# Optimization experiments

Measured on AMD Instinct MI355X. Metric: run time of the kernel, lower is better.

The kernel has to match this reference:

```python
import jax, jax.numpy as jnp
import numpy as np

GRID = 16
N = GRID * GRID          # num_nodes = 256
D = 64                   # embed_dim
SPARSITY = 0.8
BATCH = 2048


def setup_inputs() -> dict:
    key = jax.random.key(0)
    ks = jax.random.split(key, 11)
    s1 = 1.0 / np.sqrt(D)          # fan_in of per-node Linears
    s2 = 1.0 / np.sqrt(N * D)      # fan_in of global_pool first Linear
    x = jax.random.normal(ks[0], (BATCH, N * D), dtype=jnp.float32)
    adj_param = jax.random.normal(ks[1], (N, N), dtype=jnp.float32) * 0.1
    W1 = jax.random.uniform(ks[2], (N, D, D), minval=-s1, maxval=s1, dtype=jnp.float32)
    b1 = jax.random.uniform(ks[3], (N, D), minval=-s1, maxval=s1, dtype=jnp.float32)
    W2 = jax.random.uniform(ks[4], (N, D, D), minval=-s1, maxval=s1, dtype=jnp.float32)
    b2 = jax.random.uniform(ks[5], (N, D), minval=-s1, maxval=s1, dtype=jnp.float32)
    gpW1 = jax.random.uniform(ks[6], (N * D, D), minval=-s2, maxval=s2, dtype=jnp.float32)
    gpb1 = jax.random.uniform(ks[7], (D,), minval=-s2, maxval=s2, dtype=jnp.float32)
    gpW2 = jax.random.uniform(ks[8], (D, D // 2), minval=-s1, maxval=s1, dtype=jnp.float32)
    gpb2 = jax.random.uniform(ks[9], (D // 2,), minval=-s1, maxval=s1, dtype=jnp.float32)
    return {"x": x, "adj_param": adj_param, "W1": W1, "b1": b1, "W2": W2, "b2": b2,
            "gpW1": gpW1, "gpb1": gpb1, "gpW2": gpW2, "gpb2": gpb2}


def _adjacency(adj_param):
    adj = jax.nn.sigmoid(adj_param)
    # threshold = sorted(flat adj)[int(sparsity * N*N)], then hard-threshold, then zero diagonal
    thr = jnp.sort(adj.reshape(-1))[int(SPARSITY * N * N)]
    adj = adj * (adj > thr)
    return adj * (1.0 - jnp.eye(N, dtype=adj.dtype))


def reference(x, adj_param, W1, b1, W2, b2, gpW1, gpb1, gpW2, gpb2):
    B = x.shape[0]
    adj = _adjacency(adj_param)
    xn = x.reshape(B, N, D)                                    # [B, N, D]
    # per-node distinct MLP == grouped GEMM with weights [N, D, D]
    h = jax.nn.relu(jnp.einsum('bnd,nde->bne', xn, W1) + b1)   # [B, N, D]
    node = jnp.einsum('bnd,nde->bne', h, W2) + b2              # [B, N, D]
    # adjacency-weighted neighbor sum: mixed[b,i] = sum_j adj[i,j] * node[b,j]
    mixed = jnp.einsum('ij,bjd->bid', adj, node)               # [B, N, D]
    final = 0.5 * mixed + 0.5 * node                           # residual mix
    g = jax.nn.relu(final.reshape(B, N * D) @ gpW1 + gpb1)     # [B, D]
    out = g @ gpW2 + gpb2                                      # [B, D//2]
    return out, adj
```

## Files before the change

### kernel.cpp

```cpp
#include <hip/hip_runtime.h>
#include <math.h>

typedef unsigned int uint;
typedef unsigned short ushort;
typedef short short8 __attribute__((ext_vector_type(8)));
typedef float f32x4 __attribute__((ext_vector_type(4)));

#define B_ 2048
#define N_ 256
#define D_ 64
#define ND_ 16384
#define NN_ 65536
#define KIDX_ 52428u
#define NGROUPS 32

#define WS_W1T    ((size_t)0)
#define WS_W2T    ((size_t)2*1024*1024)
#define WS_EFF    ((size_t)4*1024*1024)
#define WS_GPARTS ((size_t)8*1024*1024)
#define WS_SCAL   ((size_t)24*1024*1024)

__device__ __forceinline__ ushort f2bf(float f) {
    uint u = __float_as_uint(f);
    u += 0x7fffu + ((u >> 16) & 1u);
    return (ushort)(u >> 16);
}
__device__ __forceinline__ float bf2f(ushort u) { return __uint_as_float(((uint)u) << 16); }

__device__ __forceinline__ float sigmoid_exact(float a) {
    float t = (float)exp(-(double)a);
    return 1.0f / (1.0f + t);
}

__device__ __forceinline__ int wfrag_off(int e, int k) {
    return ((((e >> 4) * 2 + (k >> 5)) * 4 + ((k >> 3) & 3)) * 16 + (e & 15)) * 8 + (k & 7);
}

__device__ __forceinline__ int afrag_off(int jl, int i) {
    return (((((jl >> 4) * 8 + (i >> 5)) * 4 + ((i >> 3) & 3)) * 16) + (jl & 15)) * 8 + (i & 7);
}

__global__ __launch_bounds__(1024) void k_cvt_radix(const float* __restrict__ W1,
                                                    const float* __restrict__ W2,
                                                    const float* __restrict__ adj_param,
                                                    ushort* __restrict__ W1f,
                                                    ushort* __restrict__ W2f,
                                                    uint* __restrict__ scal) {
    __shared__ uint SH[16390] __attribute__((aligned(16)));
    int bid = blockIdx.x, tid = threadIdx.x;

    if (bid != 0) {
        int q = tid >> 8, t = tid & 255;
        int m = (bid - 1) * 4 + q;
        ushort* P = (ushort*)SH + q * 4096;
        const float* src = (m < 256) ? W1 + (size_t)m * 4096 : W2 + (size_t)(m - 256) * 4096;
#pragma unroll
        for (int i = 0; i < 16; i++) {
            int idx = i * 256 + t;
            int k = idx >> 6, e = idx & 63;
            P[wfrag_off(e, k)] = f2bf(src[idx]);
        }
        __syncthreads();
        ushort* dst = (m < 256) ? W1f + (size_t)m * 4096 : W2f + (size_t)(m - 256) * 4096;
#pragma unroll
        for (int i = 0; i < 2; i++)
            ((uint4*)dst)[i * 256 + t] = ((const uint4*)P)[i * 256 + t];
        return;
    }

    uint* histL = SH;
    uint* wsum = SH + 16384;
    uint* bc = SH + 16388;
    int lane = tid & 63;
    uint prefix = 0;
    uint rank = KIDX_;
    const uint4* pv = (const uint4*)adj_param;
#pragma unroll 1
    for (int pass = 0; pass < 4; pass++) {
        int shift = 24 - 8 * pass;
        for (int i = tid; i < 256 * 64; i += 1024) histL[i] = 0u;
        __syncthreads();
#pragma unroll 1
        for (int i = 0; i < 16; i++) {
            uint4 b4 = pv[i * 1024 + tid];
#pragma unroll
            for (int c = 0; c < 4; c++) {
                uint bits = (c == 0) ? b4.x : (c == 1) ? b4.y : (c == 2) ? b4.z : b4.w;
                uint key = bits ^ ((bits & 0x80000000u) ? 0xFFFFFFFFu : 0x80000000u);
                bool cand = (pass == 0) || ((key >> (32 - 8 * pass)) == prefix);
                if (cand) atomicAdd(&histL[(((key >> shift) & 0xffu) << 6) + lane], 1u);
            }
        }
        __syncthreads();
        uint s0 = 0, sc = 0;
        if (tid < 256) {
#pragma unroll
            for (int l = 0; l < 64; l++) s0 += histL[(tid << 6) + ((l + tid) & 63)];
            sc = s0;
#pragma unroll
            for (int o = 1; o < 64; o <<= 1) {
                uint t2 = __shfl_up(sc, o, 64);
                if ((tid & 63) >= o) sc += t2;
            }
            if ((tid & 63) == 63) wsum[tid >> 6] = sc;
        }
        __syncthreads();
        if (tid < 256) {
            uint base = 0;
#pragma unroll
            for (int w = 0; w < 4; w++)
                if (w < (tid >> 6)) base += wsum[w];
            uint incl = base + sc;
            uint excl = incl - s0;
            if (excl <= rank && rank < incl) {
                bc[0] = (prefix << 8) | (uint)tid;
                bc[1] = rank - excl;
            }
        }
        __syncthreads();
        prefix = bc[0];
        rank = bc[1];
        __syncthreads();
    }
    if (tid == 0) {
        uint key = prefix;
        uint bits = (key & 0x80000000u) ? (key ^ 0x80000000u) : ~key;
        scal[0] = __float_as_uint(sigmoid_exact(__uint_as_float(bits)));
    }
}

__global__ __launch_bounds__(256) void k_threff(const float* __restrict__ adj_param,
                                                const uint* __restrict__ scal,
                                                const float* __restrict__ gpW1,
                                                float* __restrict__ adj_out,
                                                ushort* __restrict__ effF) {
    __shared__ ushort adjS[16384] __attribute__((aligned(16)));
    __shared__ ushort Bf[16384] __attribute__((aligned(16)));
    int d = blockIdx.x, jt = blockIdx.y, tid = threadIdx.x;
    float thr = __uint_as_float(scal[0]);

    {
        int jl = tid & 63;
        int jglob = jt * 64 + jl;
        int wrow = tid >> 6;
#pragma unroll 1
        for (int i = 0; i < 16; i++) {
            float p[4];
#pragma unroll
            for (int u = 0; u < 4; u++)
                p[u] = adj_param[(size_t)((i * 4 + u) * 4 + wrow) * 256 + jglob];
#pragma unroll
            for (int u = 0; u < 4; u++) {
                int ir = (i * 4 + u) * 4 + wrow;
                float s = sigmoid_exact(p[u]);
                float v = (s > thr && ir != jglob) ? s : 0.0f;
                adjS[afrag_off(jl, ir)] = f2bf(v);
                if (d == 0) adj_out[(size_t)ir * 256 + jglob] = v;
            }
        }
    }
#pragma unroll
    for (int t = 0; t < 16; t++) {
        int idx = t * 256 + tid;
        int i = idx >> 4;
        int f4 = idx & 15;
        float4 v = *(const float4*)(gpW1 + ((size_t)i * 64 + d) * 64 + f4 * 4);
        int slab = i >> 6, il = i & 63, e0 = f4 * 4;
        Bf[slab * 4096 + wfrag_off(e0 + 0, il)] = f2bf(v.x);
        Bf[slab * 4096 + wfrag_off(e0 + 1, il)] = f2bf(v.y);
        Bf[slab * 4096 + wfrag_off(e0 + 2, il)] = f2bf(v.z);
        Bf[slab * 4096 + wfrag_off(e0 + 3, il)] = f2bf(v.w);
    }
    __syncthreads();
    int wid = tid >> 6, lane = tid & 63, quad = lane >> 4, l16 = lane & 15;
    f32x4 acc[4];
#pragma unroll
    for (int nt = 0; nt < 4; nt++) acc[nt] = (f32x4){0.f, 0.f, 0.f, 0.f};
#pragma unroll
    for (int ks8 = 0; ks8 < 8; ks8++) {
        short8 af = *(const short8*)&adjS[((((wid * 8 + ks8) * 4 + quad) * 16 + l16)) * 8];
        int slab = ks8 >> 1, ks = ks8 & 1;
#pragma unroll
        for (int nt = 0; nt < 4; nt++) {
            short8 bf = *(const short8*)&Bf[slab * 4096 + (((nt * 2 + ks) * 4 + quad) * 16 + l16) * 8];
            acc[nt] = __builtin_amdgcn_mfma_f32_16x16x32_bf16(af, bf, acc[nt], 0, 0, 0);
        }
    }
#pragma unroll
    for (int nt = 0; nt < 4; nt++) {
        int e = nt * 16 + l16;
#pragma unroll
        for (int r = 0; r < 4; r++) {
            int j = jt * 64 + wid * 16 + quad * 4 + r;
            float w = gpW1[((size_t)j * 64 + d) * 64 + e];
            float eff = 0.5f * (acc[nt][r] + w);
            effF[(size_t)j * 4096 + wfrag_off(e, d)] = f2bf(eff);
        }
    }
}

__global__ __launch_bounds__(256, 4) void k_fused(const float* __restrict__ x,
                                                  const ushort* __restrict__ W1f,
                                                  const ushort* __restrict__ W2f,
                                                  const ushort* __restrict__ effF,
                                                  const float* __restrict__ b1,
                                                  const float* __restrict__ b2,
                                                  float* __restrict__ gparts) {
    __shared__ ushort Wf1[4096] __attribute__((aligned(16)));
    __shared__ ushort Wf2[4096] __attribute__((aligned(16)));
    __shared__ ushort Ef[4096] __attribute__((aligned(16)));
    __shared__ ushort St[4][16 * 72];
    int tid = threadIdx.x;
    int g = blockIdx.x, bt = blockIdx.y;
    int wid = tid >> 6, lane = tid & 63, quad = lane >> 4, l16 = lane & 15;
    int rbase = bt * 64 + wid * 16;
    ushort* Sw = &St[wid][0];
    const float* xrow = x + (size_t)(rbase + l16) * ND_ + quad * 8;

    int n0 = g * 8;
    uint4 w1a = ((const uint4*)(W1f + (size_t)n0 * 4096))[tid];
    uint4 w1b = ((const uint4*)(W1f + (size_t)n0 * 4096))[256 + tid];
    uint4 w2a = ((const uint4*)(W2f + (size_t)n0 * 4096))[tid];
    uint4 w2b = ((const uint4*)(W2f + (size_t)n0 * 4096))[256 + tid];
    uint4 ea  = ((const uint4*)(effF + (size_t)n0 * 4096))[tid];
    uint4 eb  = ((const uint4*)(effF + (size_t)n0 * 4096))[256 + tid];
    float4 xr0, xr1, xr2, xr3;
    {
        const float* xp = xrow + (size_t)n0 * 64;
        xr0 = *(const float4*)(xp);
        xr1 = *(const float4*)(xp + 4);
        xr2 = *(const float4*)(xp + 32);
        xr3 = *(const float4*)(xp + 36);
    }
    float b1n[4], b2n[4];
#pragma unroll
    for (int nt = 0; nt < 4; nt++) {
        b1n[nt] = b1[n0 * 64 + nt * 16 + l16];
        b2n[nt] = b2[n0 * 64 + nt * 16 + l16];
    }
    ((uint4*)Wf1)[tid] = w1a;  ((uint4*)Wf1)[256 + tid] = w1b;
    ((uint4*)Wf2)[tid] = w2a;  ((uint4*)Wf2)[256 + tid] = w2b;
    ((uint4*)Ef)[tid]  = ea;   ((uint4*)Ef)[256 + tid]  = eb;

    f32x4 accg[4];
#pragma unroll
    for (int nt = 0; nt < 4; nt++) accg[nt] = (f32x4){0.f, 0.f, 0.f, 0.f};

    __syncthreads();

#pragma unroll 1
    for (int nl = 0; nl < 8; nl++) {
        short8 fa0, fa1;
        {
            short8 a;
            a[0] = (short)f2bf(xr0.x); a[1] = (short)f2bf(xr0.y);
            a[2] = (short)f2bf(xr0.z); a[3] = (short)f2bf(xr0.w);
            a[4] = (short)f2bf(xr1.x); a[5] = (short)f2bf(xr1.y);
            a[6] = (short)f2bf(xr1.z); a[7] = (short)f2bf(xr1.w);
            fa0 = a;
            short8 b;
            b[0] = (short)f2bf(xr2.x); b[1] = (short)f2bf(xr2.y);
            b[2] = (short)f2bf(xr2.z); b[3] = (short)f2bf(xr2.w);
            b[4] = (short)f2bf(xr3.x); b[5] = (short)f2bf(xr3.y);
            b[6] = (short)f2bf(xr3.z); b[7] = (short)f2bf(xr3.w);
            fa1 = b;
        }
        float bias1[4], bias2[4];
#pragma unroll
        for (int nt = 0; nt < 4; nt++) { bias1[nt] = b1n[nt]; bias2[nt] = b2n[nt]; }

        if (nl < 7) {
            int nn = g * 8 + nl + 1;
            w1a = ((const uint4*)(W1f + (size_t)nn * 4096))[tid];
            w1b = ((const uint4*)(W1f + (size_t)nn * 4096))[256 + tid];
            w2a = ((const uint4*)(W2f + (size_t)nn * 4096))[tid];
            w2b = ((const uint4*)(W2f + (size_t)nn * 4096))[256 + tid];
            ea  = ((const uint4*)(effF + (size_t)nn * 4096))[tid];
            eb  = ((const uint4*)(effF + (size_t)nn * 4096))[256 + tid];
            const float* xp = xrow + (size_t)nn * 64;
            xr0 = *(const float4*)(xp);
            xr1 = *(const float4*)(xp + 4);
            xr2 = *(const float4*)(xp + 32);
            xr3 = *(const float4*)(xp + 36);
#pragma unroll
            for (int nt = 0; nt < 4; nt++) {
                b1n[nt] = b1[nn * 64 + nt * 16 + l16];
                b2n[nt] = b2[nn * 64 + nt * 16 + l16];
            }
        }

        f32x4 acc[4];
#pragma unroll
        for (int nt = 0; nt < 4; nt++) acc[nt] = (f32x4){0.f, 0.f, 0.f, 0.f};
#pragma unroll
        for (int nt = 0; nt < 4; nt++) {
            short8 bf = *(const short8*)&Wf1[(((nt * 2 + 0) * 4 + quad) * 16 + l16) * 8];
            acc[nt] = __builtin_amdgcn_mfma_f32_16x16x32_bf16(fa0, bf, acc[nt], 0, 0, 0);
        }
#pragma unroll
        for (int nt = 0; nt < 4; nt++) {
            short8 bf = *(const short8*)&Wf1[(((nt * 2 + 1) * 4 + quad) * 16 + l16) * 8];
            acc[nt] = __builtin_amdgcn_mfma_f32_16x16x32_bf16(fa1, bf, acc[nt], 0, 0, 0);
        }
#pragma unroll
        for (int nt = 0; nt < 4; nt++)
#pragma unroll
            for (int r = 0; r < 4; r++) {
                float h = fmaxf(acc[nt][r] + bias1[nt], 0.0f);
                Sw[(quad * 4 + r) * 72 + nt * 16 + l16] = f2bf(h);
            }
        f32x4 acc2[4];
#pragma unroll
        for (int nt = 0; nt < 4; nt++) acc2[nt] = (f32x4){0.f, 0.f, 0.f, 0.f};
#pragma unroll
        for (int ks = 0; ks < 2; ks++) {
            short8 a2 = *(const short8*)&Sw[l16 * 72 + ks * 32 + quad * 8];
#pragma unroll
            for (int nt = 0; nt < 4; nt++) {
                short8 bf = *(const short8*)&Wf2[(((nt * 2 + ks) * 4 + quad) * 16 + l16) * 8];
                acc2[nt] = __builtin_amdgcn_mfma_f32_16x16x32_bf16(a2, bf, acc2[nt], 0, 0, 0);
            }
        }
#pragma unroll
        for (int nt = 0; nt < 4; nt++)
#pragma unroll
            for (int r = 0; r < 4; r++) {
                float v = acc2[nt][r] + bias2[nt];
                Sw[(quad * 4 + r) * 72 + nt * 16 + l16] = f2bf(v);
            }
#pragma unroll
        for (int ks = 0; ks < 2; ks++) {
            short8 a3 = *(const short8*)&Sw[l16 * 72 + ks * 32 + quad * 8];
#pragma unroll
            for (int nt = 0; nt < 4; nt++) {
                short8 bf = *(const short8*)&Ef[(((nt * 2 + ks) * 4 + quad) * 16 + l16) * 8];
                accg[nt] = __builtin_amdgcn_mfma_f32_16x16x32_bf16(a3, bf, accg[nt], 0, 0, 0);
            }
        }

        if (nl < 7) {
            __syncthreads();
            ((uint4*)Wf1)[tid] = w1a;  ((uint4*)Wf1)[256 + tid] = w1b;
            ((uint4*)Wf2)[tid] = w2a;  ((uint4*)Wf2)[256 + tid] = w2b;
            ((uint4*)Ef)[tid]  = ea;   ((uint4*)Ef)[256 + tid]  = eb;
            __syncthreads();
        }
    }

    float* gp = gparts + ((size_t)g * B_ + bt * 64) * 64;
#pragma unroll
    for (int nt = 0; nt < 4; nt++)
#pragma unroll
        for (int r = 0; r < 4; r++) {
            int b_loc = wid * 16 + quad * 4 + r;
            int e = nt * 16 + l16;
            gp[b_loc * 64 + e] = accg[nt][r];
        }
}

__global__ __launch_bounds__(256) void k_gp2(const float* __restrict__ gparts,
                                             const float* __restrict__ gpb1,
                                             const float* __restrict__ gpW2,
                                             const float* __restrict__ gpb2,
                                             float* __restrict__ out) {
    __shared__ float gs[4][64];
    int b0 = blockIdx.x * 4, tid = threadIdx.x;
    int r = tid >> 6, e = tid & 63;
    float s = gpb1[e];
#pragma unroll
    for (int p = 0; p < NGROUPS; p++)
        s += gparts[((size_t)p * B_ + b0 + r) * 64 + e];
    gs[r][e] = fmaxf(s, 0.0f);
    __syncthreads();
    if (tid < 128) {
        int rr = tid >> 5, o = tid & 31;
        float a = gpb2[o];
#pragma unroll 8
        for (int k2 = 0; k2 < 64; k2++) a += gs[rr][k2] * gpW2[k2 * 32 + o];
        out[(size_t)(b0 + rr) * 32 + o] = a;
    }
}

extern "C" void kernel_launch(void* const* d_in, const int* in_sizes, int n_in,
                              void* d_out, int out_size, void* d_ws, size_t ws_size,
                              hipStream_t stream) {
    const float* x = (const float*)d_in[0];
    const float* adj_param = (const float*)d_in[1];
    const float* W1 = (const float*)d_in[2];
    const float* b1 = (const float*)d_in[3];
    const float* W2 = (const float*)d_in[4];
    const float* b2 = (const float*)d_in[5];
    const float* gpW1 = (const float*)d_in[6];
    const float* gpb1 = (const float*)d_in[7];
    const float* gpW2 = (const float*)d_in[8];
    const float* gpb2 = (const float*)d_in[9];

    float* out = (float*)d_out;
    float* adj_out = (float*)d_out + NN_;

    char* ws = (char*)d_ws;
    ushort* W1f = (ushort*)(ws + WS_W1T);
    ushort* W2f = (ushort*)(ws + WS_W2T);
    ushort* effF = (ushort*)(ws + WS_EFF);
    float* gparts = (float*)(ws + WS_GPARTS);
    uint* scal = (uint*)(ws + WS_SCAL);

    k_cvt_radix<<<129, 1024, 0, stream>>>(W1, W2, adj_param, W1f, W2f, scal);
    k_threff<<<dim3(64, 4), 256, 0, stream>>>(adj_param, scal, gpW1, adj_out, effF);
    k_fused<<<dim3(NGROUPS, 32), 256, 0, stream>>>(x, W1f, W2f, effF, b1, b2, gparts);
    k_gp2<<<512, 256, 0, stream>>>(gparts, gpb1, gpW2, gpb2, out);
}
```

Baseline: 280.4 us.

## Read per-node MFMA weight fragments directly from global instead of LDS staging

The fused kernel no longer stages each node's W1, W2 and effective-pool weight fragments through shared memory. Each wave now loads its bf16 B-fragments straight from global memory, relying on L1/L2 to serve the copies that the four waves share. This removes the two block barriers and the LDS store traffic on every node iteration, and roughly halves shared-memory use. Biases for the block's eight nodes are loaded into shared memory once up front. The trade-off is redundant global/L1 traffic per wave, and the next node's weights are no longer prefetched, so their load latency is exposed unless other waves hide it.

Result: slower. 288.7 us (+2.9%).

```diff
diff --git a/kernel.cpp b/kernel.cpp
--- a/kernel.cpp
+++ b/kernel.cpp
@@ -206,10 +206,8 @@
                                                   const float* __restrict__ b1,
                                                   const float* __restrict__ b2,
                                                   float* __restrict__ gparts) {
-    __shared__ ushort Wf1[4096] __attribute__((aligned(16)));
-    __shared__ ushort Wf2[4096] __attribute__((aligned(16)));
-    __shared__ ushort Ef[4096] __attribute__((aligned(16)));
     __shared__ ushort St[4][16 * 72];
+    __shared__ float Bs[2][8][64];
     int tid = threadIdx.x;
     int g = blockIdx.x, bt = blockIdx.y;
     int wid = tid >> 6, lane = tid & 63, quad = lane >> 4, l16 = lane & 15;
@@ -217,30 +215,25 @@
     ushort* Sw = &St[wid][0];
     const float* xrow = x + (size_t)(rbase + l16) * ND_ + quad * 8;
 
-    int n0 = g * 8;
-    uint4 w1a = ((const uint4*)(W1f + (size_t)n0 * 4096))[tid];
-    uint4 w1b = ((const uint4*)(W1f + (size_t)n0 * 4096))[256 + tid];
-    uint4 w2a = ((const uint4*)(W2f + (size_t)n0 * 4096))[tid];
-    uint4 w2b = ((const uint4*)(W2f + (size_t)n0 * 4096))[256 + tid];
-    uint4 ea  = ((const uint4*)(effF + (size_t)n0 * 4096))[tid];
-    uint4 eb  = ((const uint4*)(effF + (size_t)n0 * 4096))[256 + tid];
+    {
+        const float* b1g = b1 + (size_t)g * 512;
+        const float* b2g = b2 + (size_t)g * 512;
+        ((float*)Bs[0])[tid] = b1g[tid];
+        ((float*)Bs[0])[256 + tid] = b1g[256 + tid];
+        ((float*)Bs[1])[tid] = b2g[tid];
+        ((float*)Bs[1])[256 + tid] = b2g[256 + tid];
+    }
+
+    int lo = quad * 128 + l16 * 8;
+
     float4 xr0, xr1, xr2, xr3;
     {
-        const float* xp = xrow + (size_t)n0 * 64;
+        const float* xp = xrow + (size_t)(g * 8) * 64;
         xr0 = *(const float4*)(xp);
         xr1 = *(const float4*)(xp + 4);
         xr2 = *(const float4*)(xp + 32);
         xr3 = *(const float4*)(xp + 36);
     }
-    float b1n[4], b2n[4];
-#pragma unroll
-    for (int nt = 0; nt < 4; nt++) {
-        b1n[nt] = b1[n0 * 64 + nt * 16 + l16];
-        b2n[nt] = b2[n0 * 64 + nt * 16 + l16];
-    }
-    ((uint4*)Wf1)[tid] = w1a;  ((uint4*)Wf1)[256 + tid] = w1b;
-    ((uint4*)Wf2)[tid] = w2a;  ((uint4*)Wf2)[256 + tid] = w2b;
-    ((uint4*)Ef)[tid]  = ea;   ((uint4*)Ef)[256 + tid]  = eb;
 
     f32x4 accg[4];
 #pragma unroll
@@ -250,6 +243,11 @@
 
 #pragma unroll 1
     for (int nl = 0; nl < 8; nl++) {
+        int n = g * 8 + nl;
+        const ushort* W1n = W1f + (size_t)n * 4096 + lo;
+        const ushort* W2n = W2f + (size_t)n * 4096 + lo;
+        const ushort* Efn = effF + (size_t)n * 4096 + lo;
+
         short8 fa0, fa1;
         {
             short8 a;
@@ -265,28 +263,19 @@
             b[6] = (short)f2bf(xr3.z); b[7] = (short)f2bf(xr3.w);
             fa1 = b;
         }
-        float bias1[4], bias2[4];
-#pragma unroll
-        for (int nt = 0; nt < 4; nt++) { bias1[nt] = b1n[nt]; bias2[nt] = b2n[nt]; }
-
         if (nl < 7) {
-            int nn = g * 8 + nl + 1;
-            w1a = ((const uint4*)(W1f + (size_t)nn * 4096))[tid];
-            w1b = ((const uint4*)(W1f + (size_t)nn * 4096))[256 + tid];
-            w2a = ((const uint4*)(W2f + (size_t)nn * 4096))[tid];
-            w2b = ((const uint4*)(W2f + (size_t)nn * 4096))[256 + tid];
-            ea  = ((const uint4*)(effF + (size_t)nn * 4096))[tid];
-            eb  = ((const uint4*)(effF + (size_t)nn * 4096))[256 + tid];
-            const float* xp = xrow + (size_t)nn * 64;
+            const float* xp = xrow + (size_t)(n + 1) * 64;
             xr0 = *(const float4*)(xp);
             xr1 = *(const float4*)(xp + 4);
             xr2 = *(const float4*)(xp + 32);
             xr3 = *(const float4*)(xp + 36);
-#pragma unroll
-            for (int nt = 0; nt < 4; nt++) {
-                b1n[nt] = b1[nn * 64 + nt * 16 + l16];
-                b2n[nt] = b2[nn * 64 + nt * 16 + l16];
-            }
+        }
+
+        float bias1[4], bias2[4];
+#pragma unroll
+        for (int nt = 0; nt < 4; nt++) {
+            bias1[nt] = Bs[0][nl][nt * 16 + l16];
+            bias2[nt] = Bs[1][nl][nt * 16 + l16];
         }
 
         f32x4 acc[4];
@@ -294,12 +283,12 @@
         for (int nt = 0; nt < 4; nt++) acc[nt] = (f32x4){0.f, 0.f, 0.f, 0.f};
 #pragma unroll
         for (int nt = 0; nt < 4; nt++) {
-            short8 bf = *(const short8*)&Wf1[(((nt * 2 + 0) * 4 + quad) * 16 + l16) * 8];
+            short8 bf = *(const short8*)(W1n + nt * 1024);
             acc[nt] = __builtin_amdgcn_mfma_f32_16x16x32_bf16(fa0, bf, acc[nt], 0, 0, 0);
         }
 #pragma unroll
         for (int nt = 0; nt < 4; nt++) {
-            short8 bf = *(const short8*)&Wf1[(((nt * 2 + 1) * 4 + quad) * 16 + l16) * 8];
+            short8 bf = *(const short8*)(W1n + nt * 1024 + 512);
             acc[nt] = __builtin_amdgcn_mfma_f32_16x16x32_bf16(fa1, bf, acc[nt], 0, 0, 0);
         }
 #pragma unroll
@@ -317,7 +306,7 @@
             short8 a2 = *(const short8*)&Sw[l16 * 72 + ks * 32 + quad * 8];
 #pragma unroll
             for (int nt = 0; nt < 4; nt++) {
-                short8 bf = *(const short8*)&Wf2[(((nt * 2 + ks) * 4 + quad) * 16 + l16) * 8];
+                short8 bf = *(const short8*)(W2n + (nt * 2 + ks) * 512);
                 acc2[nt] = __builtin_amdgcn_mfma_f32_16x16x32_bf16(a2, bf, acc2[nt], 0, 0, 0);
             }
         }
@@ -333,17 +322,9 @@
             short8 a3 = *(const short8*)&Sw[l16 * 72 + ks * 32 + quad * 8];
 #pragma unroll
             for (int nt = 0; nt < 4; nt++) {
-                short8 bf = *(const short8*)&Ef[(((nt * 2 + ks) * 4 + quad) * 16 + l16) * 8];
+                short8 bf = *(const short8*)(Efn + (nt * 2 + ks) * 512);
                 accg[nt] = __builtin_amdgcn_mfma_f32_16x16x32_bf16(a3, bf, accg[nt], 0, 0, 0);
             }
-        }
-
-        if (nl < 7) {
-            __syncthreads();
-            ((uint4*)Wf1)[tid] = w1a;  ((uint4*)Wf1)[256 + tid] = w1b;
-            ((uint4*)Wf2)[tid] = w2a;  ((uint4*)Wf2)[256 + tid] = w2b;
-            ((uint4*)Ef)[tid]  = ea;   ((uint4*)Ef)[256 + tid]  = eb;
-            __syncthreads();
         }
     }
 
```

## Replace atomic-histogram radix select with register-resident 2-bit counting passes

Applied to the files above, without the earlier changes.

The threshold selection for the k-th element of adj_param previously ran four 8-bit radix passes, each building a 256-bin shared-memory histogram with per-lane atomics and a prefix scan. Now each thread keeps its 64 keys in registers and runs 16 passes of 2-bit digit counting, reduced with wave shuffles plus a small double-buffered shared array and a single barrier per pass. This removes the atomic contention, the repeated global reloads and the histogram scans, and shrinks shared memory. In exchange it uses more passes and more registers in the radix block.

After: 337.6 us. 1.2x slower.

```diff
diff --git a/kernel.cpp b/kernel.cpp
--- a/kernel.cpp
+++ b/kernel.cpp
@@ -32,6 +32,10 @@
     return 1.0f / (1.0f + t);
 }
 
+__device__ __forceinline__ uint f2key(uint bits) {
+    return bits ^ ((bits & 0x80000000u) ? 0xFFFFFFFFu : 0x80000000u);
+}
+
 __device__ __forceinline__ int wfrag_off(int e, int k) {
     return ((((e >> 4) * 2 + (k >> 5)) * 4 + ((k >> 3) & 3)) * 16 + (e & 15)) * 8 + (k & 7);
 }
@@ -46,7 +50,7 @@
                                                     ushort* __restrict__ W1f,
                                                     ushort* __restrict__ W2f,
                                                     uint* __restrict__ scal) {
-    __shared__ uint SH[16390] __attribute__((aligned(16)));
+    __shared__ uint SH[8200] __attribute__((aligned(16)));
     int bid = blockIdx.x, tid = threadIdx.x;
 
     if (bid != 0) {
@@ -68,62 +72,59 @@
         return;
     }
 
-    uint* histL = SH;
-    uint* wsum = SH + 16384;
-    uint* bc = SH + 16388;
-    int lane = tid & 63;
-    uint prefix = 0;
+    uint* tot = SH;
+    int wid = tid >> 6;
+    const uint4* pv = (const uint4*)adj_param;
+    uint4 A[16];
+#pragma unroll
+    for (int i = 0; i < 16; i++) A[i] = pv[i * 1024 + tid];
+#pragma unroll
+    for (int i = 0; i < 16; i++) {
+        A[i].x = f2key(A[i].x); A[i].y = f2key(A[i].y);
+        A[i].z = f2key(A[i].z); A[i].w = f2key(A[i].w);
+    }
+
+    uint pref = 0;
     uint rank = KIDX_;
-    const uint4* pv = (const uint4*)adj_param;
 #pragma unroll 1
-    for (int pass = 0; pass < 4; pass++) {
-        int shift = 24 - 8 * pass;
-        for (int i = tid; i < 256 * 64; i += 1024) histL[i] = 0u;
+    for (int p = 0; p < 16; p++) {
+        int b = 30 - 2 * p;
+        uint mask = (p == 0) ? 0u : (0xFFFFFFFFu << (b + 2));
+        uint c0 = 0, c1 = 0, c2 = 0;
+#pragma unroll
+        for (int i = 0; i < 16; i++) {
+#define CNT_(K) { uint k_ = (K); if (((k_ ^ pref) & mask) == 0u) { \
+                    uint d_ = (k_ >> b) & 3u; \
+                    c0 += (d_ == 0u); c1 += (d_ == 1u); c2 += (d_ == 2u); } }
+            CNT_(A[i].x) CNT_(A[i].y) CNT_(A[i].z) CNT_(A[i].w)
+#undef CNT_
+        }
+#pragma unroll
+        for (int o = 1; o < 64; o <<= 1) {
+            c0 += __shfl_xor(c0, o, 64);
+            c1 += __shfl_xor(c1, o, 64);
+            c2 += __shfl_xor(c2, o, 64);
+        }
+        if ((tid & 63) == 0) {
+            uint* s = tot + (p & 1) * 48 + wid * 3;
+            s[0] = c0; s[1] = c1; s[2] = c2;
+        }
         __syncthreads();
-#pragma unroll 1
-        for (int i = 0; i < 16; i++) {
-            uint4 b4 = pv[i * 1024 + tid];
-#pragma unroll
-            for (int c = 0; c < 4; c++) {
-                uint bits = (c == 0) ? b4.x : (c == 1) ? b4.y : (c == 2) ? b4.z : b4.w;
-                uint key = bits ^ ((bits & 0x80000000u) ? 0xFFFFFFFFu : 0x80000000u);
-                bool cand = (pass == 0) || ((key >> (32 - 8 * pass)) == prefix);
-                if (cand) atomicAdd(&histL[(((key >> shift) & 0xffu) << 6) + lane], 1u);
-            }
-        }
-        __syncthreads();
-        uint s0 = 0, sc = 0;
-        if (tid < 256) {
-#pragma unroll
-            for (int l = 0; l < 64; l++) s0 += histL[(tid << 6) + ((l + tid) & 63)];
-            sc = s0;
-#pragma unroll
-            for (int o = 1; o < 64; o <<= 1) {
-                uint t2 = __shfl_up(sc, o, 64);
-                if ((tid & 63) >= o) sc += t2;
-            }
-            if ((tid & 63) == 63) wsum[tid >> 6] = sc;
-        }
-        __syncthreads();
-        if (tid < 256) {
-            uint base = 0;
-#pragma unroll
-            for (int w = 0; w < 4; w++)
-                if (w < (tid >> 6)) base += wsum[w];
-            uint incl = base + sc;
-            uint excl = incl - s0;
-            if (excl <= rank && rank < incl) {
-                bc[0] = (prefix << 8) | (uint)tid;
-                bc[1] = rank - excl;
-            }
-        }
-        __syncthreads();
-        prefix = bc[0];
-        rank = bc[1];
-        __syncthreads();
+        uint t0 = 0, t1 = 0, t2 = 0;
+#pragma unroll
+        for (int w = 0; w < 16; w++) {
+            const uint* s = tot + (p & 1) * 48 + w * 3;
+            t0 += s[0]; t1 += s[1]; t2 += s[2];
+        }
+        uint digit;
+        if (rank < t0) { digit = 0u; }
+        else if (rank < t0 + t1) { digit = 1u; rank -= t0; }
+        else if (rank < t0 + t1 + t2) { digit = 2u; rank -= t0 + t1; }
+        else { digit = 3u; rank -= t0 + t1 + t2; }
+        pref |= digit << b;
     }
     if (tid == 0) {
-        uint key = prefix;
+        uint key = pref;
         uint bits = (key & 0x80000000u) ? (key ^ 0x80000000u) : ~key;
         scal[0] = __float_as_uint(sigmoid_exact(__uint_as_float(bits)));
     }
```
